# Kernel tuning notes

Hardware: AMD Instinct MI355X
Metric: run time of the kernel (lower is better)

The kernel has to match this reference:

```python
import jax, jax.numpy as jnp
import numpy as np
from jax import lax

B, C, H, W = 16, 8, 512, 512
HW = H * W
AX = int(np.floor(0.1 * HW))  # torch: int(np.floor(0.1 * H * W))
EPS = 1e-5


def roberts_kernels():
    # Two 2x2 Roberts cross kernels, OIHW layout [2,1,2,2]
    kx = np.array([[1.0, 0.0], [0.0, -1.0]], np.float32)
    ky = np.array([[0.0, 1.0], [-1.0, 0.0]], np.float32)
    return jnp.asarray(np.stack([kx, ky])[:, None])


def edge_maps(x, kernels):
    # x: [N,1,H,W] -> gradient magnitude flattened to [N, HW]
    g = lax.conv_general_dilated(
        x, kernels, window_strides=(1, 1), padding=[(0, 1), (0, 1)],
        dimension_numbers=("NCHW", "OIHW", "NCHW"))  # [N,2,H,W]
    mag = jnp.sqrt(g[:, 0] ** 2 + g[:, 1] ** 2 + 1e-12)
    return mag.reshape(x.shape[0], -1)


def setup_inputs() -> dict:
    key = jax.random.key(0)
    k1, k2 = jax.random.split(key)
    return {
        "predictions": jax.random.normal(k1, (B, C, H, W), jnp.float32),
        "target": jax.random.normal(k2, (B, C, H, W), jnp.float32),
        "alpha": jnp.ones((), jnp.float32),
        "kernels": roberts_kernels(),
    }


def _forward(predictions, target, alpha, kernels):
    N = B * C
    et_all = edge_maps(target.reshape(N, 1, H, W), kernels)       # [N,HW]
    ep_all = edge_maps(predictions.reshape(N, 1, H, W), kernels)  # [N,HW]

    # Faithful to the original: edge_T_final/edge_P_final persist across
    # the (i,j) loop, so the scatter state is carried sequentially.
    def step(carry, xs):
        etf, epf = carry
        et_i, ep_i = xs
        _, tb = lax.top_k(et_i, AX)
        etf = etf.at[tb].set(et_i[tb])
        _, pb = lax.top_k(ep_i, AX)
        epf = epf.at[pb].set(ep_i[pb])
        row = jnp.abs((etf - epf) / (etf + epf + EPS))
        return (etf, epf), row

    init = (jnp.zeros(HW, jnp.float32), jnp.zeros(HW, jnp.float32))
    _, edge = lax.scan(step, init, (et_all, ep_all))  # edge: [N,HW]
    return alpha * jnp.mean(edge)


def reference(predictions, target, alpha, kernels):
    return _forward(predictions, target, alpha, kernels)
```

## Files before the change

### kernel.cpp

```cpp
#include <hip/hip_runtime.h>
#include <stdint.h>

#define H 512
#define W 512
#define HW (H * W)
#define NIMG 128
#define AX 26214
#define NB 8192
#define CAP 12288
#define KS 3277
#define KM 240
#define SMEM_WORDS (NB + CAP + 512 + 4)
#define SMEM_BYTES (SMEM_WORDS * 4)

__device__ __forceinline__ float4 f4zero() { return make_float4(0.f, 0.f, 0.f, 0.f); }

__device__ __forceinline__ void block_select(uint32_t* hist, uint32_t* chunkSuf,
                                             volatile uint32_t* outBin,
                                             volatile uint32_t* outRank, uint32_t K) {
  int tid = threadIdx.x;
  if (tid < 512) {
    int base = tid * 16;
    uint32_t csum = 0;
#pragma unroll
    for (int k = 0; k < 16; k++) csum += hist[base + k];
    chunkSuf[tid] = csum;
  }
  __syncthreads();
  if (tid < 64) {
    uint32_t cs[8];
    uint32_t g = 0;
#pragma unroll
    for (int m = 0; m < 8; m++) { cs[m] = chunkSuf[tid * 8 + m]; g += cs[m]; }
    uint32_t v = g;
#pragma unroll
    for (int off = 1; off < 64; off <<= 1) {
      uint32_t u = __shfl_down(v, off);
      if (tid + off < 64) v += u;
    }
    uint32_t run = v - g;
    for (int m = 7; m >= 0; m--) {
      chunkSuf[tid * 8 + m] = run;
      run += cs[m];
    }
  }
  __syncthreads();
  if (tid < 512) {
    int base = tid * 16;
    uint32_t run = chunkSuf[tid];
    for (int k = 15; k >= 0; k--) {
      uint32_t h = hist[base + k];
      if (run < K && run + h >= K) {
        *outBin = (uint32_t)(base + k);
        *outRank = K - run;
      }
      run += h;
    }
  }
  __syncthreads();
}

__device__ __forceinline__ void sample_pass(const float* __restrict__ x,
                                            uint32_t* hist) {
  int tid = threadIdx.x;
  int lane_c = (tid & 127) << 2;
  int r0 = (tid >> 7) << 6;
  const bool haveE = lane_c + 4 < W;
  const float* xc = x + lane_c;
  float4 uA[2], uB[2];
  float fA[2], fB[2];
#define LDS2(k, buf)                                      \
  {                                                       \
    const float* rp = xc + (size_t)(r0 + 8 * (k)) * W;    \
    uA[buf] = *(const float4*)rp;                         \
    fA[buf] = haveE ? rp[4] : 0.f;                        \
    uB[buf] = *(const float4*)(rp + W);                   \
    fB[buf] = haveE ? rp[W + 4] : 0.f;                    \
  }
  LDS2(0, 0)
  for (int k = 0; k < 8; ++k) {
    int cb = k & 1;
    if (k < 7) LDS2(k + 1, cb ^ 1)
    float a[5] = {uA[cb].x, uA[cb].y, uA[cb].z, uA[cb].w, fA[cb]};
    float c[5] = {uB[cb].x, uB[cb].y, uB[cb].z, uB[cb].w, fB[cb]};
#pragma unroll
    for (int j = 0; j < 4; j++) {
      float g0 = a[j] - c[j + 1];
      float g1 = a[j + 1] - c[j];
      float msq = fmaf(g0, g0, fmaf(g1, g1, 1e-12f));
      atomicAdd(&hist[__float_as_uint(msq) >> 19], 1u);
    }
  }
#undef LDS2
}

template <int HIST>
__device__ __forceinline__ void full_pass(const float* __restrict__ x,
                                          uint32_t* hist, uint32_t* cand,
                                          uint32_t* sCnt, uint32_t lo,
                                          uint32_t span) {
  int tid = threadIdx.x;
  int lane_c = (tid & 127) << 2;
  int r0 = (tid >> 7) << 6;
  const bool haveE = lane_c + 4 < W;
  const float* xc = x + lane_c;

  float4 vA, vB, vC, vD;
  float eA = 0.f, eB = 0.f, eC = 0.f, eD = 0.f;
#define LDR(r, v, e)                                  \
  {                                                   \
    if ((r) < H) {                                    \
      const float* rp = xc + (size_t)(r) * W;         \
      v = *(const float4*)rp;                         \
      e = haveE ? rp[4] : 0.f;                        \
    } else { v = f4zero(); e = 0.f; }                 \
  }
  LDR(r0, vA, eA)
  LDR(r0 + 1, vB, eB)
  LDR(r0 + 2, vC, eC)
  for (int it = 0; it < 64; ++it) {
    int r = r0 + it;
    if (it < 62) { LDR(r + 3, vD, eD) } else { vD = f4zero(); eD = 0.f; }
    float a[5] = {vA.x, vA.y, vA.z, vA.w, eA};
    float c[5] = {vB.x, vB.y, vB.z, vB.w, eB};
#pragma unroll
    for (int j = 0; j < 4; j++) {
      float g0 = a[j] - c[j + 1];
      float g1 = a[j + 1] - c[j];
      float msq = fmaf(g0, g0, fmaf(g1, g1, 1e-12f));
      uint32_t bits = __float_as_uint(msq);
      uint32_t bin = bits >> 19;
      if (HIST) atomicAdd(&hist[bin], 1u);
      if (bin - lo <= span) {
        uint32_t idx = atomicAdd(sCnt, 1u);
        if (idx < CAP) cand[idx] = bits;
      }
    }
    vA = vB; eA = eB; vB = vC; eB = eC; vC = vD; eC = eD;
  }
#undef LDR
}

__global__ __launch_bounds__(1024) void selectKernel(const float* __restrict__ target,
                                                     const float* __restrict__ pred,
                                                     float* __restrict__ thr) {
  extern __shared__ uint32_t smem[];
  uint32_t* hist = smem;
  uint32_t* cand = smem + NB;
  uint32_t* chunkSuf = smem + NB + CAP;
  volatile uint32_t* sBin = smem + NB + CAP + 512;
  volatile uint32_t* sRank = smem + NB + CAP + 513;
  uint32_t* sCnt = smem + NB + CAP + 514;

  int tid = threadIdx.x;
  int b = blockIdx.x;
  int img = b & 127;
  const float* __restrict__ x = ((b >> 7) ? pred : target) + (size_t)img * HW;

  for (int i = tid; i < NB; i += 1024) hist[i] = 0;
  if (tid == 0) *sCnt = 0;
  __syncthreads();

  sample_pass(x, hist);
  __syncthreads();
  block_select(hist, chunkSuf, sBin, sRank, KS - KM);
  uint32_t bHi = *sBin;
  block_select(hist, chunkSuf, sBin, sRank, KS + KM);
  uint32_t bLo = *sBin;
  __syncthreads();

  for (int i = tid; i < NB; i += 1024) hist[i] = 0;
  __syncthreads();

  full_pass<1>(x, hist, cand, sCnt, bLo, bHi - bLo);
  __syncthreads();
  block_select(hist, chunkSuf, sBin, sRank, AX);
  uint32_t b0 = *sBin;
  uint32_t K1 = *sRank;
  uint32_t cnt = *sCnt;
  __syncthreads();

  bool bad = (b0 < bLo) || (b0 > bHi) || (cnt > CAP);
  if (bad) {
    if (tid == 0) *sCnt = 0;
    __syncthreads();
    full_pass<0>(x, hist, cand, sCnt, b0, 0);
    __syncthreads();
    cnt = *sCnt;
    __syncthreads();
  }
  if (cnt > CAP) cnt = CAP;

  for (int i = tid; i < NB; i += 1024) hist[i] = 0;
  __syncthreads();
  for (uint32_t j = tid; j < cnt; j += 1024) {
    uint32_t bits = cand[j];
    if ((bits >> 19) == b0) atomicAdd(&hist[(bits >> 6) & 0x1FFFu], 1u);
  }
  __syncthreads();
  block_select(hist, chunkSuf, sBin, sRank, K1);
  uint32_t b1 = *sBin;
  uint32_t K2 = *sRank;
  __syncthreads();

  for (int i = tid; i < NB; i += 1024) hist[i] = 0;
  __syncthreads();
  for (uint32_t j = tid; j < cnt; j += 1024) {
    uint32_t bits = cand[j];
    if ((bits >> 19) == b0 && ((bits >> 6) & 0x1FFFu) == b1)
      atomicAdd(&hist[bits & 63u], 1u);
  }
  __syncthreads();
  block_select(hist, chunkSuf, sBin, sRank, K2);
  if (tid == 0) {
    uint32_t tb = (b0 << 19) | (b1 << 6) | *sBin;
    thr[b] = __uint_as_float(tb);
  }
}

__global__ __launch_bounds__(512, 4) void scanKernel(const float* __restrict__ target,
                                                     const float* __restrict__ pred,
                                                     const float* __restrict__ thr,
                                                     double* __restrict__ sum) {
  __shared__ float sT[NIMG], sP[NIMG];
  __shared__ float ws8[8];
  int tid = threadIdx.x;
  if (tid < NIMG) { sT[tid] = thr[tid]; sP[tid] = thr[NIMG + tid]; }
  __syncthreads();
  int b = blockIdx.x;
  int r = ((b & 7) << 6) + (b >> 3);
  int c = tid;
  const bool haveB = r + 1 < H;
  const bool haveE = c + 1 < W;
  size_t offA = (size_t)r * W + c;
  size_t offB = offA + W;

  float t00[2], t01[2], t10[2], t11[2];
  float p00[2], p01[2], p10[2], p11[2];

#define LOADI(i, buf)                                         \
  {                                                           \
    const float* xt = target + (size_t)(i) * HW;              \
    const float* xp = pred + (size_t)(i) * HW;                \
    t00[buf] = xt[offA];                                      \
    t01[buf] = haveE ? xt[offA + 1] : 0.f;                    \
    t10[buf] = haveB ? xt[offB] : 0.f;                        \
    t11[buf] = (haveB && haveE) ? xt[offB + 1] : 0.f;         \
    p00[buf] = xp[offA];                                      \
    p01[buf] = haveE ? xp[offA + 1] : 0.f;                    \
    p10[buf] = haveB ? xp[offB] : 0.f;                        \
    p11[buf] = (haveB && haveE) ? xp[offB + 1] : 0.f;         \
  }

  float etf = 0.f, epf = 0.f, acc = 0.f;
  LOADI(0, 0)
#pragma unroll 2
  for (int i = 0; i < NIMG; ++i) {
    int cb = i & 1;
    if (i + 1 < NIMG) LOADI(i + 1, cb ^ 1)
    float tsqT = sT[i], tsqP = sP[i];
    float g0 = t00[cb] - t11[cb];
    float g1 = t01[cb] - t10[cb];
    float msq = fmaf(g0, g0, fmaf(g1, g1, 1e-12f));
    if (msq >= tsqT) etf = sqrtf(msq);
    g0 = p00[cb] - p11[cb];
    g1 = p01[cb] - p10[cb];
    float msp = fmaf(g0, g0, fmaf(g1, g1, 1e-12f));
    if (msp >= tsqP) epf = sqrtf(msp);
    acc += fabsf((etf - epf) / (etf + epf + 1e-5f));
  }
#undef LOADI

  for (int off = 32; off; off >>= 1) acc += __shfl_down(acc, off);
  if ((tid & 63) == 0) ws8[tid >> 6] = acc;
  __syncthreads();
  if (tid == 0) {
    double s = 0.0;
#pragma unroll
    for (int k = 0; k < 8; k++) s += (double)ws8[k];
    atomicAdd(sum, s);
  }
}

__global__ void initKernel(double* __restrict__ sum) { *sum = 0.0; }

__global__ void finalKernel(const double* __restrict__ sum,
                            const float* __restrict__ alpha,
                            float* __restrict__ out) {
  out[0] = (float)((double)alpha[0] * (sum[0] / (double)((double)NIMG * (double)HW)));
}

extern "C" void kernel_launch(void* const* d_in, const int* in_sizes, int n_in,
                              void* d_out, int out_size, void* d_ws, size_t ws_size,
                              hipStream_t stream) {
  const float* pred = (const float*)d_in[0];
  const float* target = (const float*)d_in[1];
  const float* alpha = (const float*)d_in[2];

  double* d_sum = (double*)d_ws;
  float* d_thr = (float*)((char*)d_ws + 64);

  static int attrSet = 0;
  if (!attrSet) {
    hipFuncSetAttribute(reinterpret_cast<const void*>(&selectKernel),
                        hipFuncAttributeMaxDynamicSharedMemorySize, SMEM_BYTES);
    attrSet = 1;
  }

  initKernel<<<1, 1, 0, stream>>>(d_sum);
  selectKernel<<<256, 1024, SMEM_BYTES, stream>>>(target, pred, d_thr);
  scanKernel<<<512, 512, 0, stream>>>(target, pred, d_thr, d_sum);
  finalKernel<<<1, 1, 0, stream>>>(d_sum, alpha, (float*)d_out);
}
```

Baseline: 408.6 us.

## Replace full-pass histogram with ballot-compacted candidate count and widen scan per thread

The select kernel's full pass no longer builds a global atomic histogram. It counts the elements above the sampled band and compacts in-band candidates through wave ballots with a single atomic per wave. The top-level bin is then found from the candidates only, with a histogram fallback if the band misses. The scan kernel now has each thread handle two columns with float2 loads in 256-thread blocks, and the sum reset moves into the select kernel so one launch is dropped. The aim is to cut LDS atomic contention and per-element load instructions, at the cost of more registers per thread and a more complex fallback path.

```diff
diff --git a/kernel.cpp b/kernel.cpp
--- a/kernel.cpp
+++ b/kernel.cpp
@@ -10,7 +10,7 @@
 #define CAP 12288
 #define KS 3277
 #define KM 240
-#define SMEM_WORDS (NB + CAP + 512 + 4)
+#define SMEM_WORDS (NB + CAP + 512 + 8)
 #define SMEM_BYTES (SMEM_WORDS * 4)
 
 __device__ __forceinline__ float4 f4zero() { return make_float4(0.f, 0.f, 0.f, 0.f); }
@@ -94,19 +94,6 @@
 #undef LDS2
 }
 
-template <int HIST>
-__device__ __forceinline__ void full_pass(const float* __restrict__ x,
-                                          uint32_t* hist, uint32_t* cand,
-                                          uint32_t* sCnt, uint32_t lo,
-                                          uint32_t span) {
-  int tid = threadIdx.x;
-  int lane_c = (tid & 127) << 2;
-  int r0 = (tid >> 7) << 6;
-  const bool haveE = lane_c + 4 < W;
-  const float* xc = x + lane_c;
-
-  float4 vA, vB, vC, vD;
-  float eA = 0.f, eB = 0.f, eC = 0.f, eD = 0.f;
 #define LDR(r, v, e)                                  \
   {                                                   \
     if ((r) < H) {                                    \
@@ -115,6 +102,69 @@
       e = haveE ? rp[4] : 0.f;                        \
     } else { v = f4zero(); e = 0.f; }                 \
   }
+
+__device__ __forceinline__ void count_pass(const float* __restrict__ x,
+                                           uint32_t* cand, uint32_t* sCnt,
+                                           uint32_t* sAbove, uint32_t loBits,
+                                           uint32_t hiBits) {
+  int tid = threadIdx.x;
+  int lane = tid & 63;
+  int lane_c = (tid & 127) << 2;
+  int r0 = (tid >> 7) << 6;
+  const bool haveE = lane_c + 4 < W;
+  const float* xc = x + lane_c;
+  uint32_t above = 0;
+
+  float4 vA, vB, vC, vD;
+  float eA = 0.f, eB = 0.f, eC = 0.f, eD = 0.f;
+  LDR(r0, vA, eA)
+  LDR(r0 + 1, vB, eB)
+  LDR(r0 + 2, vC, eC)
+  for (int it = 0; it < 64; ++it) {
+    int r = r0 + it;
+    if (it < 62) { LDR(r + 3, vD, eD) } else { vD = f4zero(); eD = 0.f; }
+    float a[5] = {vA.x, vA.y, vA.z, vA.w, eA};
+    float c[5] = {vB.x, vB.y, vB.z, vB.w, eB};
+#pragma unroll
+    for (int j = 0; j < 4; j++) {
+      float g0 = a[j] - c[j + 1];
+      float g1 = a[j + 1] - c[j];
+      float msq = fmaf(g0, g0, fmaf(g1, g1, 1e-12f));
+      uint32_t bits = __float_as_uint(msq);
+      above += (bits >= hiBits) ? 1u : 0u;
+      bool w = (bits >= loBits) && (bits < hiBits);
+      unsigned long long mk = __ballot(w);
+      if (mk) {
+        uint32_t base = 0;
+        int leader = __ffsll(mk) - 1;
+        uint32_t pre = (uint32_t)__popcll(mk & ((1ull << lane) - 1ull));
+        if (lane == leader) base = atomicAdd(sCnt, (uint32_t)__popcll(mk));
+        base = (uint32_t)__shfl((int)base, leader);
+        if (w) {
+          uint32_t idx = base + pre;
+          if (idx < CAP) cand[idx] = bits;
+        }
+      }
+    }
+    vA = vB; eA = eB; vB = vC; eB = eC; vC = vD; eC = eD;
+  }
+  for (int off = 32; off; off >>= 1) above += __shfl_down(above, off);
+  if (lane == 0) atomicAdd(sAbove, above);
+}
+
+template <int HIST>
+__device__ __forceinline__ void full_pass(const float* __restrict__ x,
+                                          uint32_t* hist, uint32_t* cand,
+                                          uint32_t* sCnt, uint32_t lo,
+                                          uint32_t span) {
+  int tid = threadIdx.x;
+  int lane_c = (tid & 127) << 2;
+  int r0 = (tid >> 7) << 6;
+  const bool haveE = lane_c + 4 < W;
+  const float* xc = x + lane_c;
+
+  float4 vA, vB, vC, vD;
+  float eA = 0.f, eB = 0.f, eC = 0.f, eD = 0.f;
   LDR(r0, vA, eA)
   LDR(r0 + 1, vB, eB)
   LDR(r0 + 2, vC, eC)
@@ -138,12 +188,13 @@
     }
     vA = vB; eA = eB; vB = vC; eB = eC; vC = vD; eC = eD;
   }
+}
 #undef LDR
-}
 
 __global__ __launch_bounds__(1024) void selectKernel(const float* __restrict__ target,
                                                      const float* __restrict__ pred,
-                                                     float* __restrict__ thr) {
+                                                     float* __restrict__ thr,
+                                                     double* __restrict__ sum) {
   extern __shared__ uint32_t smem[];
   uint32_t* hist = smem;
   uint32_t* cand = smem + NB;
@@ -151,14 +202,16 @@
   volatile uint32_t* sBin = smem + NB + CAP + 512;
   volatile uint32_t* sRank = smem + NB + CAP + 513;
   uint32_t* sCnt = smem + NB + CAP + 514;
+  uint32_t* sAbove = smem + NB + CAP + 515;
 
   int tid = threadIdx.x;
   int b = blockIdx.x;
+  if (b == 0 && tid == 0) *sum = 0.0;
   int img = b & 127;
   const float* __restrict__ x = ((b >> 7) ? pred : target) + (size_t)img * HW;
 
   for (int i = tid; i < NB; i += 1024) hist[i] = 0;
-  if (tid == 0) *sCnt = 0;
+  if (tid == 0) { *sCnt = 0; *sAbove = 0; }
   __syncthreads();
 
   sample_pass(x, hist);
@@ -169,27 +222,42 @@
   uint32_t bLo = *sBin;
   __syncthreads();
 
-  for (int i = tid; i < NB; i += 1024) hist[i] = 0;
-  __syncthreads();
-
-  full_pass<1>(x, hist, cand, sCnt, bLo, bHi - bLo);
-  __syncthreads();
-  block_select(hist, chunkSuf, sBin, sRank, AX);
-  uint32_t b0 = *sBin;
-  uint32_t K1 = *sRank;
+  uint32_t loBits = bLo << 19;
+  uint32_t hiBits = (bHi >= 8191u) ? 0xFFFFFFFFu : ((bHi + 1u) << 19);
+  count_pass(x, cand, sCnt, sAbove, loBits, hiBits);
+  __syncthreads();
   uint32_t cnt = *sCnt;
-  __syncthreads();
-
-  bool bad = (b0 < bLo) || (b0 > bHi) || (cnt > CAP);
-  if (bad) {
+  uint32_t above = *sAbove;
+  __syncthreads();
+
+  uint32_t b0, K1;
+  bool ok = (above < AX) && ((AX - above) <= cnt) && (cnt <= CAP);
+  if (ok) {
+    for (int i = tid; i < NB; i += 1024) hist[i] = 0;
+    __syncthreads();
+    for (uint32_t j = tid; j < cnt; j += 1024)
+      atomicAdd(&hist[cand[j] >> 19], 1u);
+    __syncthreads();
+    block_select(hist, chunkSuf, sBin, sRank, AX - above);
+    b0 = *sBin;
+    K1 = *sRank;
+    __syncthreads();
+  } else {
+    for (int i = tid; i < NB; i += 1024) hist[i] = 0;
+    __syncthreads();
+    full_pass<1>(x, hist, cand, sCnt, 0xFFFFFFFFu, 0u);
+    __syncthreads();
+    block_select(hist, chunkSuf, sBin, sRank, AX);
+    b0 = *sBin;
+    K1 = *sRank;
     if (tid == 0) *sCnt = 0;
     __syncthreads();
-    full_pass<0>(x, hist, cand, sCnt, b0, 0);
+    full_pass<0>(x, hist, cand, sCnt, b0, 0u);
     __syncthreads();
     cnt = *sCnt;
-    __syncthreads();
-  }
-  if (cnt > CAP) cnt = CAP;
+    if (cnt > CAP) cnt = CAP;
+    __syncthreads();
+  }
 
   for (int i = tid; i < NB; i += 1024) hist[i] = 0;
   __syncthreads();
@@ -218,71 +286,77 @@
   }
 }
 
-__global__ __launch_bounds__(512, 4) void scanKernel(const float* __restrict__ target,
-                                                     const float* __restrict__ pred,
-                                                     const float* __restrict__ thr,
-                                                     double* __restrict__ sum) {
+__global__ __launch_bounds__(256) void scanKernel(const float* __restrict__ target,
+                                                  const float* __restrict__ pred,
+                                                  const float* __restrict__ thr,
+                                                  double* __restrict__ sum) {
   __shared__ float sT[NIMG], sP[NIMG];
-  __shared__ float ws8[8];
-  int tid = threadIdx.x;
-  if (tid < NIMG) { sT[tid] = thr[tid]; sP[tid] = thr[NIMG + tid]; }
+  __shared__ float ws4[4];
+  int tid = threadIdx.x;
+  if (tid < NIMG) sT[tid] = thr[tid];
+  else if (tid < 2 * NIMG) sP[tid - NIMG] = thr[tid];
   __syncthreads();
   int b = blockIdx.x;
   int r = ((b & 7) << 6) + (b >> 3);
-  int c = tid;
+  int c = tid << 1;
   const bool haveB = r + 1 < H;
-  const bool haveE = c + 1 < W;
+  const bool haveE = c + 2 < W;
   size_t offA = (size_t)r * W + c;
   size_t offB = offA + W;
 
-  float t00[2], t01[2], t10[2], t11[2];
-  float p00[2], p01[2], p10[2], p11[2];
-
-#define LOADI(i, buf)                                         \
-  {                                                           \
-    const float* xt = target + (size_t)(i) * HW;              \
-    const float* xp = pred + (size_t)(i) * HW;                \
-    t00[buf] = xt[offA];                                      \
-    t01[buf] = haveE ? xt[offA + 1] : 0.f;                    \
-    t10[buf] = haveB ? xt[offB] : 0.f;                        \
-    t11[buf] = (haveB && haveE) ? xt[offB + 1] : 0.f;         \
-    p00[buf] = xp[offA];                                      \
-    p01[buf] = haveE ? xp[offA + 1] : 0.f;                    \
-    p10[buf] = haveB ? xp[offB] : 0.f;                        \
-    p11[buf] = (haveB && haveE) ? xp[offB + 1] : 0.f;         \
-  }
-
-  float etf = 0.f, epf = 0.f, acc = 0.f;
+  float2 tA[2], tB[2], pA[2], pB[2];
+  float tAe[2], tBe[2], pAe[2], pBe[2];
+
+#define LOADI(i, buf)                                                  \
+  {                                                                    \
+    const float* xt = target + (size_t)(i) * HW;                       \
+    const float* xp = pred + (size_t)(i) * HW;                         \
+    tA[buf] = *(const float2*)(xt + offA);                             \
+    pA[buf] = *(const float2*)(xp + offA);                             \
+    tB[buf] = haveB ? *(const float2*)(xt + offB) : make_float2(0.f, 0.f); \
+    pB[buf] = haveB ? *(const float2*)(xp + offB) : make_float2(0.f, 0.f); \
+    tAe[buf] = haveE ? xt[offA + 2] : 0.f;                             \
+    pAe[buf] = haveE ? xp[offA + 2] : 0.f;                             \
+    tBe[buf] = (haveE && haveB) ? xt[offB + 2] : 0.f;                  \
+    pBe[buf] = (haveE && haveB) ? xp[offB + 2] : 0.f;                  \
+  }
+
+  float etf0 = 0.f, etf1 = 0.f, epf0 = 0.f, epf1 = 0.f, acc = 0.f;
   LOADI(0, 0)
 #pragma unroll 2
   for (int i = 0; i < NIMG; ++i) {
     int cb = i & 1;
     if (i + 1 < NIMG) LOADI(i + 1, cb ^ 1)
     float tsqT = sT[i], tsqP = sP[i];
-    float g0 = t00[cb] - t11[cb];
-    float g1 = t01[cb] - t10[cb];
-    float msq = fmaf(g0, g0, fmaf(g1, g1, 1e-12f));
-    if (msq >= tsqT) etf = sqrtf(msq);
-    g0 = p00[cb] - p11[cb];
-    g1 = p01[cb] - p10[cb];
-    float msp = fmaf(g0, g0, fmaf(g1, g1, 1e-12f));
-    if (msp >= tsqP) epf = sqrtf(msp);
-    acc += fabsf((etf - epf) / (etf + epf + 1e-5f));
+    float g0 = tA[cb].x - tB[cb].y;
+    float g1 = tA[cb].y - tB[cb].x;
+    float m = fmaf(g0, g0, fmaf(g1, g1, 1e-12f));
+    if (m >= tsqT) etf0 = sqrtf(m);
+    g0 = pA[cb].x - pB[cb].y;
+    g1 = pA[cb].y - pB[cb].x;
+    m = fmaf(g0, g0, fmaf(g1, g1, 1e-12f));
+    if (m >= tsqP) epf0 = sqrtf(m);
+    acc += fabsf((etf0 - epf0) / (etf0 + epf0 + 1e-5f));
+    g0 = tA[cb].y - tBe[cb];
+    g1 = tAe[cb] - tB[cb].y;
+    m = fmaf(g0, g0, fmaf(g1, g1, 1e-12f));
+    if (m >= tsqT) etf1 = sqrtf(m);
+    g0 = pA[cb].y - pBe[cb];
+    g1 = pAe[cb] - pB[cb].y;
+    m = fmaf(g0, g0, fmaf(g1, g1, 1e-12f));
+    if (m >= tsqP) epf1 = sqrtf(m);
+    acc += fabsf((etf1 - epf1) / (etf1 + epf1 + 1e-5f));
   }
 #undef LOADI
 
   for (int off = 32; off; off >>= 1) acc += __shfl_down(acc, off);
-  if ((tid & 63) == 0) ws8[tid >> 6] = acc;
+  if ((tid & 63) == 0) ws4[tid >> 6] = acc;
   __syncthreads();
   if (tid == 0) {
-    double s = 0.0;
-#pragma unroll
-    for (int k = 0; k < 8; k++) s += (double)ws8[k];
+    double s = (double)ws4[0] + (double)ws4[1] + (double)ws4[2] + (double)ws4[3];
     atomicAdd(sum, s);
   }
 }
-
-__global__ void initKernel(double* __restrict__ sum) { *sum = 0.0; }
 
 __global__ void finalKernel(const double* __restrict__ sum,
                             const float* __restrict__ alpha,
@@ -307,8 +381,7 @@
     attrSet = 1;
   }
 
-  initKernel<<<1, 1, 0, stream>>>(d_sum);
-  selectKernel<<<256, 1024, SMEM_BYTES, stream>>>(target, pred, d_thr);
-  scanKernel<<<512, 512, 0, stream>>>(target, pred, d_thr, d_sum);
+  selectKernel<<<256, 1024, SMEM_BYTES, stream>>>(target, pred, d_thr, d_sum);
+  scanKernel<<<512, 256, 0, stream>>>(target, pred, d_thr, d_sum);
   finalKernel<<<1, 1, 0, stream>>>(d_sum, alpha, (float*)d_out);
 }
```

Measured after the change: 438.4 us. +7.3%, slower.
